# Kernel tuning notes

Measured on AMD Instinct MI355X. Metric: run time of the kernel, lower is better.

Reference implementation:

```python
import jax, jax.numpy as jnp
import numpy as np
from jax import lax

B, T, C_IN, HW = 16, 2048, 17, 8
N_CONV, HID, OUT = 4, 150, 2
IN_SZ = N_CONV * 6 * 6  # 144


def setup_inputs() -> dict:
    key = jax.random.key(0)
    ks = jax.random.split(key, 9)
    s = lambda *sh: 1.0 / np.sqrt(sh[-1])
    return {
        "inputs": jax.random.normal(ks[0], (B, T, C_IN, HW, HW), jnp.float32),
        "conv_w": jax.random.normal(ks[1], (N_CONV, C_IN, 3, 3), jnp.float32) * 0.1,
        "conv_b": jax.random.normal(ks[2], (N_CONV,), jnp.float32) * 0.1,
        "w_ih": jax.random.normal(ks[3], (4 * HID, IN_SZ), jnp.float32) * s(IN_SZ),
        "w_hh": jax.random.normal(ks[4], (4 * HID, HID), jnp.float32) * s(HID),
        "b_ih": jax.random.normal(ks[5], (4 * HID,), jnp.float32) * s(HID),
        "b_hh": jax.random.normal(ks[6], (4 * HID,), jnp.float32) * s(HID),
        "last_w": jax.random.normal(ks[7], (OUT, HID), jnp.float32) * s(HID),
        "last_b": jax.random.normal(ks[8], (OUT,), jnp.float32) * s(HID),
    }


def reference(inputs, conv_w, conv_b, w_ih, w_hh, b_ih, b_hh, last_w, last_b):
    b, t = inputs.shape[:2]
    # Conv2d over all timesteps at once (same math as the per-step loop).
    x = inputs.reshape(b * t, C_IN, HW, HW)
    y = lax.conv_general_dilated(
        x, conv_w, window_strides=(1, 1), padding="VALID",
        dimension_numbers=("NCHW", "OIHW", "NCHW"),
    ) + conv_b[None, :, None, None]           # [B*T, 4, 6, 6]
    y = jax.nn.relu(y).reshape(b, t, IN_SZ)   # [B, T, 144]
    # Precompute input-to-gate projection for every step (batched GEMM).
    gates_x = jnp.einsum("btf,gf->btg", y, w_ih) + b_ih + b_hh  # [B, T, 600]

    def step(carry, gx):
        h, c = carry
        g = gx + h @ w_hh.T  # [B, 600]; PyTorch gate order: i, f, g, o
        i, f, gg, o = jnp.split(g, 4, axis=-1)
        c = jax.nn.sigmoid(f) * c + jax.nn.sigmoid(i) * jnp.tanh(gg)
        h = jax.nn.sigmoid(o) * jnp.tanh(c)
        return (h, c), None

    h0 = jnp.zeros((b, HID), inputs.dtype)
    (hT, _), _ = lax.scan(step, (h0, h0), jnp.swapaxes(gates_x, 0, 1))
    return hT @ last_w.T + last_b  # [B, 2] == last(h_T).squeeze()
```

## Files before the change

### kernel.cpp

```cpp
#include <hip/hip_runtime.h>

typedef _Float16 f16;
typedef _Float16 f16x4 __attribute__((ext_vector_type(4)));
typedef _Float16 f16x8 __attribute__((ext_vector_type(8)));
typedef float f32x4 __attribute__((ext_vector_type(4)));
typedef int i32x4 __attribute__((ext_vector_type(4)));

#define TLEN 2048
#define TPAD 2050
#define NCOL 640
#define GSTEP (16 * NCOL)
#define K1   1.4426950408889634f
#define K2   2.8853900817779268f

__global__ __launch_bounds__(64) void rowmax_k(const float* __restrict__ w_hh,
                                               float* __restrict__ rowmax)
{
    const int r = blockIdx.x * 64 + threadIdx.x;
    if (r < 600) {
        float m = 0.f;
        for (int k = 0; k < 150; ++k) m = fmaxf(m, fabsf(w_hh[r * 150 + k]));
        rowmax[r] = m;
    }
}

__global__ void prep_weights(const float* __restrict__ w_ih,
                             const float* __restrict__ w_hh,
                             const float* __restrict__ b_ih,
                             const float* __restrict__ b_hh,
                             const float* __restrict__ rowmax,
                             f16* __restrict__ wihf, signed char* __restrict__ whhq,
                             float* __restrict__ biasp, float* __restrict__ dsc)
{
    const int idx = blockIdx.x * blockDim.x + threadIdx.x;
    const int stride = gridDim.x * blockDim.x;
    for (int i = idx; i < 40 * 5 * 64 * 8; i += stride) {
        const int e = i & 7;
        const int lane = (i >> 3) & 63;
        const int kt = (i >> 9) % 5;
        const int nt = i / 2560;
        const int colg = nt * 16 + (lane & 15);
        const int u = colg >> 2, G = colg & 3;
        const int k = kt * 32 + (lane >> 4) * 8 + e;
        const float sc = (G == 2) ? K2 : -K1;
        f16 vi = (f16)0.f;
        if (u < 150 && k < 144) vi = (f16)(w_ih[(G * 150 + u) * 144 + k] * sc);
        wihf[i] = vi;
    }
    for (int i = idx; i < 40 * 3 * 64 * 16; i += stride) {
        const int byte = i & 15;
        const int lane = (i >> 4) & 63;
        const int kt = (i >> 10) % 3;
        const int nt = i / 3072;
        const int colg = nt * 16 + (lane & 15);
        const int u = colg >> 2, G = colg & 3;
        const int k = kt * 64 + (lane >> 4) * 16 + byte;
        signed char q = 0;
        if (u < 150 && k < 150) {
            const int row = G * 150 + u;
            const float rm = rowmax[row];
            if (rm > 0.f)
                q = (signed char)(int)rintf(w_hh[row * 150 + k] * (127.f / rm));
        }
        whhq[i] = q;
    }
    for (int i = idx; i < NCOL; i += stride) {
        const int u = i >> 2, G = i & 3;
        const float sc = (G == 2) ? K2 : -K1;
        biasp[i] = (u < 150) ? (b_ih[G * 150 + u] + b_hh[G * 150 + u]) * sc : 0.f;
        dsc[i]   = (u < 150) ? sc * rowmax[G * 150 + u] * (1.f / 16129.f) : 0.f;
    }
}

__global__ __launch_bounds__(256) void conv_relu(
    const float* __restrict__ in, const float* __restrict__ cw,
    const float* __restrict__ cb, f16* __restrict__ y)
{
    __shared__ float s_in[4][1088];
    __shared__ float s_w[612];
    __shared__ float s_b[4];
    const int tid = threadIdx.x, sub = tid >> 6, lt = tid & 63;
    const int bt = blockIdx.x * 4 + sub;
    const float* ip = in + (size_t)bt * 1088;
    #pragma unroll
    for (int i = 0; i < 17; ++i) s_in[sub][lt + i * 64] = ip[lt + i * 64];
    for (int i = tid; i < 612; i += 256) s_w[i] = cw[i];
    if (tid < 4) s_b[tid] = cb[tid];
    __syncthreads();
    const int b = bt >> 11, t = bt & 2047;
    f16* yr = y + (size_t)(t * 16 + b) * 160;
    for (int i = lt; i < 160; i += 64) {
        float v = 0.f;
        if (i < 144) {
            const int oc = i / 36, rr = i % 36, oy = rr / 6, ox = rr % 6;
            float acc = s_b[oc];
            const float* wp = s_w + oc * 153;
            const float* bp = &s_in[sub][oy * 8 + ox];
            #pragma unroll
            for (int ic = 0; ic < 17; ++ic)
                #pragma unroll
                for (int ky = 0; ky < 3; ++ky)
                    #pragma unroll
                    for (int kx = 0; kx < 3; ++kx)
                        acc += bp[ic * 64 + ky * 8 + kx] * wp[ic * 9 + ky * 3 + kx];
            v = fmaxf(acc, 0.f);
        }
        yr[i] = (f16)v;
    }
}

__global__ __launch_bounds__(640, 1) void gates_gemm(
    const f16* __restrict__ y, const f16* __restrict__ wihf,
    const float* __restrict__ biasp, f16* __restrict__ gates3)
{
    const int tid = threadIdx.x, wv = tid >> 6, lane = tid & 63;
    const int col = lane & 15, grp = lane >> 4;
    const int t0 = blockIdx.x * 8;

    f16x8 bfr[4][5];
    float bb[4];
    #pragma unroll
    for (int i = 0; i < 4; ++i) {
        const int nt = wv * 4 + i;
        const f16* wf = wihf + (size_t)(nt * 5) * 512;
        #pragma unroll
        for (int kt = 0; kt < 5; ++kt)
            bfr[i][kt] = *(const f16x8*)(wf + kt * 512 + lane * 8);
        bb[i] = biasp[nt * 16 + col];
    }

    for (int t = t0; t < t0 + 8; ++t) {
        f16x8 a[5];
        const f16* yr = y + (size_t)(t * 16 + col) * 160;
        #pragma unroll
        for (int kt = 0; kt < 5; ++kt)
            a[kt] = *(const f16x8*)(yr + kt * 32 + grp * 8);
        #pragma unroll
        for (int i = 0; i < 4; ++i) {
            const int nt = wv * 4 + i;
            f32x4 acc = {0.f, 0.f, 0.f, 0.f};
            #pragma unroll
            for (int kt = 0; kt < 5; ++kt)
                acc = __builtin_amdgcn_mfma_f32_16x16x32_f16(a[kt], bfr[i][kt], acc, 0, 0, 0);
            const int colg = nt * 16 + col;
            #pragma unroll
            for (int r = 0; r < 4; ++r)
                gates3[((size_t)(t * 16 + grp * 4 + r)) * NCOL + colg] = (f16)(acc[r] + bb[i]);
        }
    }
}

__device__ __forceinline__ void lstm_stepQ(
    int t, int cur, f16x4& pfu, f16x4& pfc, const f16*& pLoad,
    const i32x4 (&afrag)[5][3], const f32x4& scv,
    signed char* hqs, f16* hfs, float& cst,
    int grp, int sel, bool wr, int u)
{
    const f16x4 pnew = *(const f16x4*)pLoad;
    pLoad += GSTEP;

    const signed char* hr = hqs + cur * 192 + grp * 16;
    i32x4 bf[3];
    #pragma unroll
    for (int kt = 0; kt < 3; ++kt)
        bf[kt] = *(const i32x4*)(hr + kt * 64);

    float gx0 = (float)pfu[0], gx1 = (float)pfu[1];
    float gx2 = (float)pfu[2], gx3 = (float)pfu[3];
    pfc = pnew;

    const i32x4 zc = {0, 0, 0, 0};
    i32x4 acc[5];
    #pragma unroll
    for (int i = 0; i < 5; ++i)
        acc[i] = __builtin_amdgcn_mfma_i32_16x16x64_i8(afrag[i][0], bf[0], zc, 0, 0, 0);
    #pragma unroll
    for (int kt = 1; kt < 3; ++kt)
        #pragma unroll
        for (int i = 0; i < 5; ++i)
            acc[i] = __builtin_amdgcn_mfma_i32_16x16x64_i8(afrag[i][kt], bf[kt], acc[i], 0, 0, 0);

    int s0 = acc[0][0], s1 = acc[0][1], s2 = acc[0][2], s3 = acc[0][3];
    #pragma unroll
    for (int i = 1; i < 5; ++i) {
        const bool p = (sel == i);
        s0 = p ? acc[i][0] : s0;
        s1 = p ? acc[i][1] : s1;
        s2 = p ? acc[i][2] : s2;
        s3 = p ? acc[i][3] : s3;
    }

    const float g0 = fmaf((float)s0, scv[0], gx0);
    const float g1 = fmaf((float)s1, scv[1], gx1);
    const float g2 = fmaf((float)s2, scv[2], gx2);
    const float g3 = fmaf((float)s3, scv[3], gx3);

    const float ei = __builtin_amdgcn_exp2f(g0);
    const float ef = __builtin_amdgcn_exp2f(g1);
    const float eg = __builtin_amdgcn_exp2f(fminf(g2, 38.f));
    const float eo = __builtin_amdgcn_exp2f(g3);
    const float sig_i = __builtin_amdgcn_rcpf(1.f + ei);
    const float sig_f = __builtin_amdgcn_rcpf(1.f + ef);
    const float sig_o = __builtin_amdgcn_rcpf(1.f + eo);
    const float tng   = (eg - 1.f) * __builtin_amdgcn_rcpf(eg + 1.f);
    const float c = sig_f * cst + sig_i * tng;
    cst = c;
    const float ec = __builtin_amdgcn_exp2f(fminf(K2 * c, 80.f));
    const float tnc = (ec - 1.f) * __builtin_amdgcn_rcpf(ec + 1.f);
    const float h = sig_o * tnc;

    if (wr) hqs[(cur ^ 1) * 192 + u] = (signed char)(int)rintf(127.f * h);
    if (t == TLEN - 1 && wr) hfs[u] = (f16)h;

    asm volatile("s_waitcnt lgkmcnt(0)" ::: "memory");
    __builtin_amdgcn_s_barrier();
    __builtin_amdgcn_sched_barrier(0);
}

__global__ __launch_bounds__(512, 1) void lstm_scan(
    const f16* __restrict__ gates3, const signed char* __restrict__ whhq,
    const float* __restrict__ dsc,
    const float* __restrict__ last_w, const float* __restrict__ last_b,
    float* __restrict__ out)
{
    __shared__ __align__(16) signed char hq[2 * 192];
    __shared__ __align__(16) f16 hf[160];
    const int b = blockIdx.x;
    const int tid = threadIdx.x, w = tid >> 6, lane = tid & 63;
    const int col = lane & 15, grp = lane >> 4;
    const int sel = (col < 5) ? col : ((col < 10) ? col - 5 : ((col < 15) ? col - 10 : 0));
    const bool wr = (col < 5);
    const int u = 20 * w + 4 * sel + grp;

    for (int i = tid; i < 2 * 192; i += 512) hq[i] = 0;

    i32x4 afrag[5][3];
    #pragma unroll
    for (int i = 0; i < 5; ++i)
        #pragma unroll
        for (int kt = 0; kt < 3; ++kt)
            afrag[i][kt] =
                *(const i32x4*)(whhq + (size_t)(((5 * w + i) * 3 + kt) * 64 + lane) * 16);

    const f32x4 scv = *(const f32x4*)(dsc + 4 * u);

    float cst = 0.f;
    __syncthreads();

    const f16* gbu = gates3 + (size_t)b * NCOL + 80 * w + 16 * sel + 4 * grp;

    f16x4 pA = *(const f16x4*)(gbu);
    f16x4 pB = *(const f16x4*)(gbu + (size_t)1 * GSTEP);
    const f16* pLoad = gbu + (size_t)2 * GSTEP;

    #pragma unroll 1
    for (int tb = 0; tb < TLEN; tb += 2) {
        lstm_stepQ(tb,     0, pA, pA, pLoad, afrag, scv, hq, hf, cst, grp, sel, wr, u);
        lstm_stepQ(tb + 1, 1, pB, pB, pLoad, afrag, scv, hq, hf, cst, grp, sel, wr, u);
    }

    if (tid < 2) {
        float s = last_b[tid];
        for (int j = 0; j < 150; ++j)
            s += (float)hf[j] * last_w[tid * 150 + j];
        out[b * 2 + tid] = s;
    }
}

extern "C" void kernel_launch(void* const* d_in, const int* in_sizes, int n_in,
                              void* d_out, int out_size, void* d_ws, size_t ws_size,
                              hipStream_t stream) {
    const float* inp    = (const float*)d_in[0];
    const float* conv_w = (const float*)d_in[1];
    const float* conv_b = (const float*)d_in[2];
    const float* w_ih   = (const float*)d_in[3];
    const float* w_hh   = (const float*)d_in[4];
    const float* b_ih   = (const float*)d_in[5];
    const float* b_hh   = (const float*)d_in[6];
    const float* last_w = (const float*)d_in[7];
    const float* last_b = (const float*)d_in[8];
    float* out = (float*)d_out;

    char* ws = (char*)d_ws;
    size_t off = 0;
    f16*   y      = (f16*)(ws + off);  off += 10485760;
    f16*   gates3 = (f16*)(ws + off);  off += 41984000;
    f16*   wihf   = (f16*)(ws + off);  off += 204800;
    signed char* whhq = (signed char*)(ws + off); off += 122880;
    float* biasp  = (float*)(ws + off); off += 2560;
    float* dsc    = (float*)(ws + off); off += 2560;
    float* rowmax = (float*)(ws + off); off += 2432;

    rowmax_k<<<10, 64, 0, stream>>>(w_hh, rowmax);
    prep_weights<<<120, 256, 0, stream>>>(w_ih, w_hh, b_ih, b_hh, rowmax,
                                          wihf, whhq, biasp, dsc);
    conv_relu<<<8192, 256, 0, stream>>>(inp, conv_w, conv_b, y);
    gates_gemm<<<256, 640, 0, stream>>>(y, wihf, biasp, gates3);
    lstm_scan<<<16, 512, 0, stream>>>(gates3, whhq, dsc, last_w, last_b, out);
}
```

Before: 1.092 ms.

## Fuse conv, gate GEMM and LSTM scan into one producer-consumer kernel

Replaces the separate conv_relu, gates_gemm and lstm_scan launches with a single persistent kernel. 16 blocks run the LSTM scan while 240 producer blocks compute conv and the input-gate GEMM per 8-step chunk, publishing completion through release/acquire flags. This lets the sequential scan overlap the input preprocessing and drops the intermediate y buffer round trip. It also folds the sigmoid reciprocals into fewer rcp operations in the step math. The cost is a spin-wait dependency that assumes all 256 blocks are co-resident, plus lower producer throughput for conv, since each block now handles only 16 samples per timestep.

```diff
diff --git a/kernel.cpp b/kernel.cpp
--- a/kernel.cpp
+++ b/kernel.cpp
@@ -10,8 +10,10 @@
 #define TPAD 2050
 #define NCOL 640
 #define GSTEP (16 * NCOL)
-#define K1   1.4426950408889634f
-#define K2   2.8853900817779268f
+#define NPROD 240
+#define NCHUNK 256
+#define K1 1.4426950408889634f
+#define K2 2.8853900817779268f
 
 __global__ __launch_bounds__(64) void rowmax_k(const float* __restrict__ w_hh,
                                                float* __restrict__ rowmax)
@@ -72,84 +74,6 @@
     }
 }
 
-__global__ __launch_bounds__(256) void conv_relu(
-    const float* __restrict__ in, const float* __restrict__ cw,
-    const float* __restrict__ cb, f16* __restrict__ y)
-{
-    __shared__ float s_in[4][1088];
-    __shared__ float s_w[612];
-    __shared__ float s_b[4];
-    const int tid = threadIdx.x, sub = tid >> 6, lt = tid & 63;
-    const int bt = blockIdx.x * 4 + sub;
-    const float* ip = in + (size_t)bt * 1088;
-    #pragma unroll
-    for (int i = 0; i < 17; ++i) s_in[sub][lt + i * 64] = ip[lt + i * 64];
-    for (int i = tid; i < 612; i += 256) s_w[i] = cw[i];
-    if (tid < 4) s_b[tid] = cb[tid];
-    __syncthreads();
-    const int b = bt >> 11, t = bt & 2047;
-    f16* yr = y + (size_t)(t * 16 + b) * 160;
-    for (int i = lt; i < 160; i += 64) {
-        float v = 0.f;
-        if (i < 144) {
-            const int oc = i / 36, rr = i % 36, oy = rr / 6, ox = rr % 6;
-            float acc = s_b[oc];
-            const float* wp = s_w + oc * 153;
-            const float* bp = &s_in[sub][oy * 8 + ox];
-            #pragma unroll
-            for (int ic = 0; ic < 17; ++ic)
-                #pragma unroll
-                for (int ky = 0; ky < 3; ++ky)
-                    #pragma unroll
-                    for (int kx = 0; kx < 3; ++kx)
-                        acc += bp[ic * 64 + ky * 8 + kx] * wp[ic * 9 + ky * 3 + kx];
-            v = fmaxf(acc, 0.f);
-        }
-        yr[i] = (f16)v;
-    }
-}
-
-__global__ __launch_bounds__(640, 1) void gates_gemm(
-    const f16* __restrict__ y, const f16* __restrict__ wihf,
-    const float* __restrict__ biasp, f16* __restrict__ gates3)
-{
-    const int tid = threadIdx.x, wv = tid >> 6, lane = tid & 63;
-    const int col = lane & 15, grp = lane >> 4;
-    const int t0 = blockIdx.x * 8;
-
-    f16x8 bfr[4][5];
-    float bb[4];
-    #pragma unroll
-    for (int i = 0; i < 4; ++i) {
-        const int nt = wv * 4 + i;
-        const f16* wf = wihf + (size_t)(nt * 5) * 512;
-        #pragma unroll
-        for (int kt = 0; kt < 5; ++kt)
-            bfr[i][kt] = *(const f16x8*)(wf + kt * 512 + lane * 8);
-        bb[i] = biasp[nt * 16 + col];
-    }
-
-    for (int t = t0; t < t0 + 8; ++t) {
-        f16x8 a[5];
-        const f16* yr = y + (size_t)(t * 16 + col) * 160;
-        #pragma unroll
-        for (int kt = 0; kt < 5; ++kt)
-            a[kt] = *(const f16x8*)(yr + kt * 32 + grp * 8);
-        #pragma unroll
-        for (int i = 0; i < 4; ++i) {
-            const int nt = wv * 4 + i;
-            f32x4 acc = {0.f, 0.f, 0.f, 0.f};
-            #pragma unroll
-            for (int kt = 0; kt < 5; ++kt)
-                acc = __builtin_amdgcn_mfma_f32_16x16x32_f16(a[kt], bfr[i][kt], acc, 0, 0, 0);
-            const int colg = nt * 16 + col;
-            #pragma unroll
-            for (int r = 0; r < 4; ++r)
-                gates3[((size_t)(t * 16 + grp * 4 + r)) * NCOL + colg] = (f16)(acc[r] + bb[i]);
-        }
-    }
-}
-
 __device__ __forceinline__ void lstm_stepQ(
     int t, int cur, f16x4& pfu, f16x4& pfc, const f16*& pLoad,
     const i32x4 (&afrag)[5][3], const f32x4& scv,
@@ -199,15 +123,12 @@
     const float ef = __builtin_amdgcn_exp2f(g1);
     const float eg = __builtin_amdgcn_exp2f(fminf(g2, 38.f));
     const float eo = __builtin_amdgcn_exp2f(g3);
-    const float sig_i = __builtin_amdgcn_rcpf(1.f + ei);
-    const float sig_f = __builtin_amdgcn_rcpf(1.f + ef);
-    const float sig_o = __builtin_amdgcn_rcpf(1.f + eo);
-    const float tng   = (eg - 1.f) * __builtin_amdgcn_rcpf(eg + 1.f);
-    const float c = sig_f * cst + sig_i * tng;
+    const float dig = (1.f + ei) * (eg + 1.f);
+    const float c = cst * __builtin_amdgcn_rcpf(1.f + ef)
+                  + (eg - 1.f) * __builtin_amdgcn_rcpf(dig);
     cst = c;
     const float ec = __builtin_amdgcn_exp2f(fminf(K2 * c, 80.f));
-    const float tnc = (ec - 1.f) * __builtin_amdgcn_rcpf(ec + 1.f);
-    const float h = sig_o * tnc;
+    const float h = (ec - 1.f) * __builtin_amdgcn_rcpf((1.f + eo) * (ec + 1.f));
 
     if (wr) hqs[(cur ^ 1) * 192 + u] = (signed char)(int)rintf(127.f * h);
     if (t == TLEN - 1 && wr) hfs[u] = (f16)h;
@@ -217,17 +138,109 @@
     __builtin_amdgcn_sched_barrier(0);
 }
 
-__global__ __launch_bounds__(512, 1) void lstm_scan(
-    const f16* __restrict__ gates3, const signed char* __restrict__ whhq,
-    const float* __restrict__ dsc,
+__global__ __launch_bounds__(512, 1) void mega(
+    const float* __restrict__ inp, const float* __restrict__ cw,
+    const float* __restrict__ cb,
+    const f16* __restrict__ wihf, const float* __restrict__ biasp,
+    f16* __restrict__ gates3,
+    const signed char* __restrict__ whhq, const float* __restrict__ dsc,
     const float* __restrict__ last_w, const float* __restrict__ last_b,
-    float* __restrict__ out)
+    int* __restrict__ flags, float* __restrict__ out)
 {
+    const int bid = blockIdx.x;
+    const int tid = threadIdx.x, w = tid >> 6, lane = tid & 63;
+    const int col = lane & 15, grp = lane >> 4;
+
+    if (bid >= 16) {
+        __shared__ float s_in[16][1092];
+        __shared__ __align__(16) f16 s_y[8][16][168];
+        __shared__ float s_w[612];
+        for (int i = tid; i < 612; i += 512) s_w[i] = cw[i];
+
+        f16x8 bfr[5][5];
+        float bb[5];
+        #pragma unroll
+        for (int i = 0; i < 5; ++i) {
+            const int nt = w * 5 + i;
+            const f16* wf = wihf + (size_t)(nt * 5) * 512;
+            #pragma unroll
+            for (int kt = 0; kt < 5; ++kt)
+                bfr[i][kt] = *(const f16x8*)(wf + kt * 512 + lane * 8);
+            bb[i] = biasp[nt * 16 + col];
+        }
+        const int cb_b = tid & 15, unit = tid >> 4;
+        const int oc = unit / 6, oy = unit % 6;
+        const float cbias = (unit < 24) ? cb[oc] : 0.f;
+        __syncthreads();
+
+        for (int ch = bid - 16; ch < NCHUNK; ch += NPROD) {
+            const int t0 = ch * 8;
+            for (int tl = 0; tl < 8; ++tl) {
+                const int t = t0 + tl;
+                __syncthreads();
+                {
+                    const int si = tid >> 5, l2 = tid & 31;
+                    const float* ip = inp + ((size_t)si * TLEN + t) * 1088;
+                    for (int k = l2; k < 1088; k += 32) s_in[si][k] = ip[k];
+                }
+                __syncthreads();
+                if (unit < 24) {
+                    const float* wp = s_w + oc * 153;
+                    float acc[6] = {cbias, cbias, cbias, cbias, cbias, cbias};
+                    #pragma unroll 1
+                    for (int ic = 0; ic < 17; ++ic) {
+                        const float* rowb = &s_in[cb_b][ic * 64 + oy * 8];
+                        #pragma unroll
+                        for (int ky = 0; ky < 3; ++ky) {
+                            const float* r = rowb + ky * 8;
+                            const float w0 = wp[ic * 9 + ky * 3 + 0];
+                            const float w1 = wp[ic * 9 + ky * 3 + 1];
+                            const float w2 = wp[ic * 9 + ky * 3 + 2];
+                            #pragma unroll
+                            for (int ox = 0; ox < 6; ++ox)
+                                acc[ox] += r[ox] * w0 + r[ox + 1] * w1 + r[ox + 2] * w2;
+                        }
+                    }
+                    #pragma unroll
+                    for (int ox = 0; ox < 6; ++ox)
+                        s_y[tl][cb_b][oc * 36 + oy * 6 + ox] = (f16)fmaxf(acc[ox], 0.f);
+                } else if (unit == 24) {
+                    #pragma unroll
+                    for (int k = 0; k < 16; ++k) s_y[tl][cb_b][144 + k] = (f16)0.f;
+                }
+            }
+            __syncthreads();
+            for (int tl = 0; tl < 8; ++tl) {
+                const int t = t0 + tl;
+                f16x8 a[5];
+                #pragma unroll
+                for (int kt = 0; kt < 5; ++kt)
+                    a[kt] = *(const f16x8*)(&s_y[tl][col][kt * 32 + grp * 8]);
+                #pragma unroll
+                for (int i = 0; i < 5; ++i) {
+                    f32x4 acc = {0.f, 0.f, 0.f, 0.f};
+                    #pragma unroll
+                    for (int kt = 0; kt < 5; ++kt)
+                        acc = __builtin_amdgcn_mfma_f32_16x16x32_f16(a[kt], bfr[i][kt], acc, 0, 0, 0);
+                    const int colg = (w * 5 + i) * 16 + col;
+                    #pragma unroll
+                    for (int r = 0; r < 4; ++r)
+                        gates3[((size_t)(t * 16 + grp * 4 + r)) * NCOL + colg] =
+                            (f16)(acc[r] + bb[i]);
+                }
+            }
+            __threadfence();
+            __syncthreads();
+            if (tid == 0)
+                __hip_atomic_store(&flags[ch], 1, __ATOMIC_RELEASE,
+                                   __HIP_MEMORY_SCOPE_AGENT);
+        }
+        return;
+    }
+
     __shared__ __align__(16) signed char hq[2 * 192];
     __shared__ __align__(16) f16 hf[160];
-    const int b = blockIdx.x;
-    const int tid = threadIdx.x, w = tid >> 6, lane = tid & 63;
-    const int col = lane & 15, grp = lane >> 4;
+    const int b = bid;
     const int sel = (col < 5) ? col : ((col < 10) ? col - 5 : ((col < 15) ? col - 10 : 0));
     const bool wr = (col < 5);
     const int u = 20 * w + 4 * sel + grp;
@@ -243,18 +256,33 @@
                 *(const i32x4*)(whhq + (size_t)(((5 * w + i) * 3 + kt) * 64 + lane) * 16);
 
     const f32x4 scv = *(const f32x4*)(dsc + 4 * u);
-
     float cst = 0.f;
     __syncthreads();
 
+    while (__hip_atomic_load(&flags[0], __ATOMIC_ACQUIRE, __HIP_MEMORY_SCOPE_AGENT) == 0)
+        __builtin_amdgcn_s_sleep(2);
+    int pend = __hip_atomic_load(&flags[1], __ATOMIC_ACQUIRE, __HIP_MEMORY_SCOPE_AGENT);
+
     const f16* gbu = gates3 + (size_t)b * NCOL + 80 * w + 16 * sel + 4 * grp;
-
     f16x4 pA = *(const f16x4*)(gbu);
     f16x4 pB = *(const f16x4*)(gbu + (size_t)1 * GSTEP);
     const f16* pLoad = gbu + (size_t)2 * GSTEP;
 
     #pragma unroll 1
     for (int tb = 0; tb < TLEN; tb += 2) {
+        const int tn = tb + 2;
+        if ((tn & 7) == 0 && tn < TLEN) {
+            const int ch = tn >> 3;
+            while (pend == 0) {
+                pend = __hip_atomic_load(&flags[ch], __ATOMIC_ACQUIRE,
+                                         __HIP_MEMORY_SCOPE_AGENT);
+                if (!pend) __builtin_amdgcn_s_sleep(2);
+            }
+            pend = (ch + 1 < NCHUNK)
+                 ? __hip_atomic_load(&flags[ch + 1], __ATOMIC_ACQUIRE,
+                                     __HIP_MEMORY_SCOPE_AGENT)
+                 : 1;
+        }
         lstm_stepQ(tb,     0, pA, pA, pLoad, afrag, scv, hq, hf, cst, grp, sel, wr, u);
         lstm_stepQ(tb + 1, 1, pB, pB, pLoad, afrag, scv, hq, hf, cst, grp, sel, wr, u);
     }
@@ -283,18 +311,18 @@
 
     char* ws = (char*)d_ws;
     size_t off = 0;
-    f16*   y      = (f16*)(ws + off);  off += 10485760;
-    f16*   gates3 = (f16*)(ws + off);  off += 41984000;
+    f16*   gates3 = (f16*)(ws + off);  off += (size_t)TPAD * 16 * NCOL * 2;
     f16*   wihf   = (f16*)(ws + off);  off += 204800;
     signed char* whhq = (signed char*)(ws + off); off += 122880;
     float* biasp  = (float*)(ws + off); off += 2560;
     float* dsc    = (float*)(ws + off); off += 2560;
-    float* rowmax = (float*)(ws + off); off += 2432;
-
+    float* rowmax = (float*)(ws + off); off += 2560;
+    int*   flags  = (int*)(ws + off);   off += (NCHUNK + 4) * 4;
+
+    hipMemsetAsync(flags, 0, (NCHUNK + 4) * 4, stream);
     rowmax_k<<<10, 64, 0, stream>>>(w_hh, rowmax);
     prep_weights<<<120, 256, 0, stream>>>(w_ih, w_hh, b_ih, b_hh, rowmax,
                                           wihf, whhq, biasp, dsc);
-    conv_relu<<<8192, 256, 0, stream>>>(inp, conv_w, conv_b, y);
-    gates_gemm<<<256, 640, 0, stream>>>(y, wihf, biasp, gates3);
-    lstm_scan<<<16, 512, 0, stream>>>(gates3, whhq, dsc, last_w, last_b, out);
-}
+    mega<<<256, 512, 0, stream>>>(inp, conv_w, conv_b, wihf, biasp, gates3,
+                                  whhq, dsc, last_w, last_b, flags, out);
+}
```

Measured after the change: 1.234 ms. 1.13x slower.
